# Kernel optimization log

Hardware: AMD Instinct MI355X
Metric: run time of the kernel (lower is better)

The kernel has to match this reference:

```python
import jax, jax.numpy as jnp
import numpy as np

B, L, D, H, HS, V, NL = 8, 513, 512, 8, 64, 513, 6  # head_size = D // H
EPS = 1e-5


def setup_inputs() -> dict:
    key = jax.random.key(0)
    ks = jax.random.split(key, 8)
    s = 0.02
    return {
        "x": jax.random.randint(ks[0], (B, L), 0, V),
        "embed": jax.random.normal(ks[1], (V, D), jnp.float32) * s,
        "pos_embed": jax.random.normal(ks[2], (L, D), jnp.float32) * s,
        "Wq": jax.random.normal(ks[3], (NL, H, D, HS), jnp.float32) * s,
        "Wk": jax.random.normal(ks[4], (NL, H, D, HS), jnp.float32) * s,
        "Wv": jax.random.normal(ks[5], (NL, H, D, HS), jnp.float32) * s,
        "ln1_g": jnp.ones((NL, D), jnp.float32),
        "ln1_b": jnp.zeros((NL, D), jnp.float32),
        "ln2_g": jnp.ones((NL, D), jnp.float32),
        "ln2_b": jnp.zeros((NL, D), jnp.float32),
        "mlp_W": jax.random.normal(ks[6], (NL, D, D), jnp.float32) * s,
        "mlp_b": jnp.zeros((NL, D), jnp.float32),
        "fc_W": jax.random.normal(ks[7], (D, V), jnp.float32) * s,
        "fc_b": jnp.zeros((V,), jnp.float32),
    }


def _layernorm(x, g, b):
    mu = jnp.mean(x, axis=-1, keepdims=True)
    var = jnp.mean(jnp.square(x - mu), axis=-1, keepdims=True)
    return (x - mu) * jax.lax.rsqrt(var + EPS) * g + b


def reference(x, embed, pos_embed, Wq, Wk, Wv, ln1_g, ln1_b, ln2_g, ln2_b,
              mlp_W, mlp_b, fc_W, fc_b):
    h = embed[x] + pos_embed[None]                       # (B, L, D)
    mask = jnp.tril(jnp.ones((L, L), bool))              # causal tril buffer
    scale = HS ** -0.5
    for i in range(NL):
        xn = _layernorm(h, ln1_g[i], ln1_b[i])
        # all heads batched (original loops per head; same math)
        q = jnp.einsum('bld,hde->bhle', xn, Wq[i])
        k = jnp.einsum('bld,hde->bhle', xn, Wk[i])
        v = jnp.einsum('bld,hde->bhle', xn, Wv[i])
        w = jnp.einsum('bhle,bhme->bhlm', q, k) * scale
        w = jnp.where(mask, w, -jnp.inf)
        w = jax.nn.softmax(w, axis=-1)
        y = jnp.einsum('bhlm,bhme->bhle', w, v)
        y = y.transpose(0, 2, 1, 3).reshape(B, L, D)     # concat heads
        h = y + h
        xn2 = _layernorm(h, ln2_g[i], ln2_b[i])
        h = jax.nn.gelu(xn2 @ mlp_W[i] + mlp_b[i], approximate=False) + h
    return h @ fc_W + fc_b                               # (B, L, V) logits
```

## Files before the change

### kernel.cpp

```cpp
#include <hip/hip_runtime.h>
#include <hip/hip_bf16.h>
#include <math.h>

#define B 8
#define L 513
#define D 512
#define H 8
#define HS 64
#define V 513
#define NL 6
#define BL (B * L)
#define LP 576
#define EPS 1e-5f

typedef __attribute__((ext_vector_type(8))) short bf16x8;
typedef __attribute__((ext_vector_type(4))) float f32x4;

__device__ inline ushort f2b(float f) {
    __hip_bfloat16 h = __float2bfloat16(f);
    return *reinterpret_cast<ushort*>(&h);
}

__global__ __launch_bounds__(256) void embed_k(const int* __restrict__ x,
                                               const float* __restrict__ emb,
                                               const float* __restrict__ pos,
                                               float* __restrict__ hbuf)
{
    int row = blockIdx.x;
    int l   = row % L;
    int tok = x[row];
    const float* er = emb + (size_t)tok * D;
    const float* pr = pos + (size_t)l * D;
    float* hr = hbuf + (size_t)row * D;
    for (int d = threadIdx.x; d < D; d += 256)
        hr[d] = er[d] + pr[d];
}

__global__ __launch_bounds__(256) void ln_k(const float* __restrict__ x,
                                            const float* __restrict__ g,
                                            const float* __restrict__ b,
                                            ushort* __restrict__ o)
{
    const int row = blockIdx.x, tid = threadIdx.x;
    const float* xr = x + (size_t)row * D;
    float v0 = xr[tid], v1 = xr[tid + 256];
    __shared__ float red[256];
    red[tid] = v0 + v1;
    __syncthreads();
    for (int off = 128; off > 0; off >>= 1) {
        if (tid < off) red[tid] += red[tid + off];
        __syncthreads();
    }
    float mu = red[0] * (1.f / D);
    __syncthreads();
    float d0 = v0 - mu, d1 = v1 - mu;
    red[tid] = d0 * d0 + d1 * d1;
    __syncthreads();
    for (int off = 128; off > 0; off >>= 1) {
        if (tid < off) red[tid] += red[tid + off];
        __syncthreads();
    }
    float rs = rsqrtf(red[0] * (1.f / D) + EPS);
    ushort* orow = o + (size_t)row * D;
    orow[tid]       = f2b(d0 * rs * g[tid]       + b[tid]);
    orow[tid + 256] = f2b(d1 * rs * g[tid + 256] + b[tid + 256]);
}

__global__ __launch_bounds__(256) void h2bf_k(const float* __restrict__ h,
                                              ushort* __restrict__ o)
{
    int idx = blockIdx.x * 256 + threadIdx.x;
    float4 f = *(const float4*)(h + (size_t)idx * 4);
    ushort4 u;
    u.x = f2b(f.x); u.y = f2b(f.y); u.z = f2b(f.z); u.w = f2b(f.w);
    *(ushort4*)(o + (size_t)idx * 4) = u;
}

__global__ __launch_bounds__(256) void cvt_qkv_k(const float* __restrict__ Wq,
                                                 const float* __restrict__ Wk,
                                                 const float* __restrict__ Wv,
                                                 ushort* __restrict__ Wp)
{
    const int dc = blockIdx.x;
    const int i  = blockIdx.y / H, h = blockIdx.y % H;
    const int sel = blockIdx.z;
    const float* W = (sel == 0) ? Wq : (sel == 1) ? Wk : Wv;
    const float* src = W + ((size_t)i * H + h) * D * HS + (size_t)dc * 64 * HS;
    __shared__ float T[64][65];
    const int tid = threadIdx.x;
#pragma unroll
    for (int it = 0; it < 4; ++it) {
        int idx = tid + it * 256;
        int r = idx >> 4, e4 = (idx & 15) * 4;
        float4 f = *(const float4*)(src + (size_t)r * HS + e4);
        T[r][e4] = f.x; T[r][e4 + 1] = f.y; T[r][e4 + 2] = f.z; T[r][e4 + 3] = f.w;
    }
    __syncthreads();
    ushort* dst = Wp + (size_t)i * 1536 * 512 + (size_t)(sel * 512 + h * 64) * 512 + dc * 64;
#pragma unroll
    for (int it = 0; it < 4; ++it) {
        int idx = tid + it * 256;
        int e = idx >> 4, d4 = (idx & 15) * 4;
        ushort4 u;
        u.x = f2b(T[d4][e]); u.y = f2b(T[d4 + 1][e]);
        u.z = f2b(T[d4 + 2][e]); u.w = f2b(T[d4 + 3][e]);
        *(ushort4*)(dst + (size_t)e * 512 + d4) = u;
    }
}

__global__ __launch_bounds__(256) void cvt_mlp_k(const float* __restrict__ Wm,
                                                 ushort* __restrict__ Wt)
{
    const int nt = blockIdx.x, kt = blockIdx.y, i = blockIdx.z;
    const float* src = Wm + (size_t)i * D * D;
    __shared__ float T[64][65];
    const int tid = threadIdx.x;
#pragma unroll
    for (int it = 0; it < 4; ++it) {
        int idx = tid + it * 256;
        int r = idx >> 4, e4 = (idx & 15) * 4;
        float4 f = *(const float4*)(src + (size_t)(kt * 64 + r) * D + nt * 64 + e4);
        T[r][e4] = f.x; T[r][e4 + 1] = f.y; T[r][e4 + 2] = f.z; T[r][e4 + 3] = f.w;
    }
    __syncthreads();
    ushort* dst = Wt + (size_t)i * D * D + (size_t)(nt * 64) * D + kt * 64;
#pragma unroll
    for (int it = 0; it < 4; ++it) {
        int idx = tid + it * 256;
        int e = idx >> 4, k4 = (idx & 15) * 4;
        ushort4 u;
        u.x = f2b(T[k4][e]); u.y = f2b(T[k4 + 1][e]);
        u.z = f2b(T[k4 + 2][e]); u.w = f2b(T[k4 + 3][e]);
        *(ushort4*)(dst + (size_t)e * D + k4) = u;
    }
}

__global__ __launch_bounds__(256) void cvt_fc_k(const float* __restrict__ Wf,
                                                ushort* __restrict__ Wt)
{
    const int nt = blockIdx.x, kt = blockIdx.y;
    __shared__ float T[64][65];
    const int tid = threadIdx.x;
#pragma unroll
    for (int it = 0; it < 4; ++it) {
        int idx = tid + it * 256;
        int r = idx >> 4, e4 = (idx & 15) * 4;
#pragma unroll
        for (int j = 0; j < 4; ++j) {
            int n = nt * 64 + e4 + j;
            T[r][e4 + j] = (n < V) ? Wf[(size_t)(kt * 64 + r) * V + n] : 0.f;
        }
    }
    __syncthreads();
    ushort* dst = Wt + (size_t)(nt * 64) * 512 + kt * 64;
#pragma unroll
    for (int it = 0; it < 4; ++it) {
        int idx = tid + it * 256;
        int e = idx >> 4, k4 = (idx & 15) * 4;
        ushort4 u;
        u.x = f2b(T[k4][e]); u.y = f2b(T[k4 + 1][e]);
        u.z = f2b(T[k4 + 2][e]); u.w = f2b(T[k4 + 3][e]);
        *(ushort4*)(dst + (size_t)e * 512 + k4) = u;
    }
}

template <int MODE>
__global__ __launch_bounds__(256) void mgemm_k(const ushort* __restrict__ A,
                                               const ushort* __restrict__ Bt,
                                               const float* __restrict__ bias,
                                               void* __restrict__ o0,
                                               void* __restrict__ o1,
                                               void* __restrict__ o2)
{
    __shared__ ushort As[64][72];
    __shared__ ushort Bs[64][72];
    const int tid  = threadIdx.x;
    const int wave = tid >> 6, lane = tid & 63;
    const int row0 = blockIdx.y * 64;
    const int col0 = blockIdx.x * 64;
    const int wr = (wave >> 1) * 32, wc = (wave & 1) * 32;
    const int frow = lane & 15;
    const int kb   = lane >> 4;

    f32x4 acc[2][2] = {};

    for (int k0 = 0; k0 < 512; k0 += 64) {
#pragma unroll
        for (int it = 0; it < 2; ++it) {
            int idx = tid + it * 256;
            int r = idx >> 3, kc = idx & 7;
            uint4 av = make_uint4(0u, 0u, 0u, 0u);
            if (row0 + r < BL)
                av = *(const uint4*)(A + (size_t)(row0 + r) * 512 + k0 + kc * 8);
            *(uint4*)&As[r][kc * 8] = av;
            uint4 bv = *(const uint4*)(Bt + (size_t)(col0 + r) * 512 + k0 + kc * 8);
            *(uint4*)&Bs[r][kc * 8] = bv;
        }
        __syncthreads();
#pragma unroll
        for (int ks = 0; ks < 2; ++ks) {
            bf16x8 a[2], b[2];
#pragma unroll
            for (int f = 0; f < 2; ++f) {
                a[f] = *(const bf16x8*)&As[wr + f * 16 + frow][ks * 32 + kb * 8];
                b[f] = *(const bf16x8*)&Bs[wc + f * 16 + frow][ks * 32 + kb * 8];
            }
#pragma unroll
            for (int fi = 0; fi < 2; ++fi)
#pragma unroll
                for (int fj = 0; fj < 2; ++fj)
                    acc[fi][fj] = __builtin_amdgcn_mfma_f32_16x16x32_bf16(
                        a[fi], b[fj], acc[fi][fj], 0, 0, 0);
        }
        __syncthreads();
    }

    const int rbase = row0 + wr + (lane >> 4) * 4;
    const int cbase = col0 + wc + (lane & 15);
#pragma unroll
    for (int fi = 0; fi < 2; ++fi) {
#pragma unroll
        for (int fj = 0; fj < 2; ++fj) {
            const int c = cbase + fj * 16;
#pragma unroll
            for (int rg = 0; rg < 4; ++rg) {
                const int r = rbase + fi * 16 + rg;
                if (r >= BL) continue;
                float val = acc[fi][fj][rg];
                if (MODE == 0) {
                    int buf = c >> 9, cc = c & 511;
                    int b_ = r / L, l = r % L;
                    int head = cc >> 6, e = cc & 63;
                    int bh = b_ * H + head;
                    if (buf == 0)
                        ((ushort*)o0)[((size_t)bh * L + l) * HS + e] = f2b(val);
                    else if (buf == 1)
                        ((ushort*)o1)[((size_t)bh * L + l) * HS + e] = f2b(val);
                    else
                        ((ushort*)o2)[((size_t)bh * HS + e) * LP + l] = f2b(val);
                } else if (MODE == 1) {
                    float xv = val + bias[c];
                    float gl = 0.5f * xv * (1.f + erff(xv * 0.70710678118654752f));
                    ((float*)o0)[(size_t)r * D + c] = gl + ((float*)o0)[(size_t)r * D + c];
                } else {
                    if (c < V) ((float*)o0)[(size_t)r * V + c] = val + bias[c];
                }
            }
        }
    }
}

__global__ __launch_bounds__(256) void fattn_k(const ushort* __restrict__ qb,
                                               const ushort* __restrict__ kb,
                                               const ushort* __restrict__ vT,
                                               float* __restrict__ hbuf)
{
    __shared__ ushort Qs[64][72];
    __shared__ ushort Ks[64][72];
    __shared__ ushort Vs[64][72];
    __shared__ ushort Ps[64][72];

    const int bx  = blockIdx.x;
    const int bh  = bx / 9;
    const int qt  = 8 - (bx % 9);
    const int q0  = qt * 64;
    const int tid = threadIdx.x;
    const int wave = tid >> 6, lane = tid & 63;
    const int lg = lane >> 4, li = lane & 15;
    const int wq = wave * 16;

#pragma unroll
    for (int it = 0; it < 2; ++it) {
        int idx = tid + it * 256;
        int r = idx >> 3, c8 = (idx & 7) * 8;
        int qr = q0 + r;
        uint4 val = make_uint4(0u, 0u, 0u, 0u);
        if (qr < L) val = *(const uint4*)(qb + ((size_t)bh * L + qr) * HS + c8);
        *(uint4*)&Qs[r][c8] = val;
    }

    float m_run[4], l_run[4];
    f32x4 accO[4] = {};
#pragma unroll
    for (int rg = 0; rg < 4; ++rg) { m_run[rg] = -INFINITY; l_run[rg] = 0.f; }

    const int n_mt = qt + 1;

    for (int t = 0; t < n_mt; ++t) {
        const int m0 = t * 64;
#pragma unroll
        for (int it = 0; it < 2; ++it) {
            int idx = tid + it * 256;
            int r = idx >> 3, c8 = (idx & 7) * 8;
            int mr = m0 + r;
            uint4 kv = make_uint4(0u, 0u, 0u, 0u);
            if (mr < L) kv = *(const uint4*)(kb + ((size_t)bh * L + mr) * HS + c8);
            *(uint4*)&Ks[r][c8] = kv;
            int mc = m0 + c8;
            uint4 vv = make_uint4(0u, 0u, 0u, 0u);
            if (mc + 7 < L) {
                vv = *(const uint4*)(vT + ((size_t)bh * HS + r) * LP + mc);
            } else {
                ushort tmp[8] = {0, 0, 0, 0, 0, 0, 0, 0};
#pragma unroll
                for (int j2 = 0; j2 < 8; ++j2)
                    if (mc + j2 < L) tmp[j2] = vT[((size_t)bh * HS + r) * LP + mc + j2];
                vv = *(uint4*)tmp;
            }
            *(uint4*)&Vs[r][c8] = vv;
        }
        __syncthreads();

        f32x4 accS[4] = {};
#pragma unroll
        for (int ks = 0; ks < 2; ++ks) {
            bf16x8 a = *(const bf16x8*)&Qs[wq + li][ks * 32 + lg * 8];
#pragma unroll
            for (int j = 0; j < 4; ++j) {
                bf16x8 b = *(const bf16x8*)&Ks[j * 16 + li][ks * 32 + lg * 8];
                accS[j] = __builtin_amdgcn_mfma_f32_16x16x32_bf16(a, b, accS[j], 0, 0, 0);
            }
        }

#pragma unroll
        for (int rg = 0; rg < 4; ++rg) {
            const int qrow = q0 + wq + lg * 4 + rg;
            float sv[4];
            float rmax = -INFINITY;
#pragma unroll
            for (int j = 0; j < 4; ++j) {
                int mcol = m0 + j * 16 + li;
                float s = accS[j][rg] * 0.125f;
                if (mcol > qrow || mcol >= L) s = -INFINITY;
                sv[j] = s;
                rmax = fmaxf(rmax, s);
            }
            rmax = fmaxf(rmax, __shfl_xor(rmax, 1));
            rmax = fmaxf(rmax, __shfl_xor(rmax, 2));
            rmax = fmaxf(rmax, __shfl_xor(rmax, 4));
            rmax = fmaxf(rmax, __shfl_xor(rmax, 8));
            const float mnew = fmaxf(m_run[rg], rmax);
            const float fs = __expf(m_run[rg] - mnew);
            float psum = 0.f;
#pragma unroll
            for (int j = 0; j < 4; ++j) {
                float p = __expf(sv[j] - mnew);
                psum += p;
                Ps[wq + lg * 4 + rg][j * 16 + li] = f2b(p);
            }
            psum += __shfl_xor(psum, 1);
            psum += __shfl_xor(psum, 2);
            psum += __shfl_xor(psum, 4);
            psum += __shfl_xor(psum, 8);
            l_run[rg] = l_run[rg] * fs + psum;
            m_run[rg] = mnew;
#pragma unroll
            for (int j = 0; j < 4; ++j) accO[j][rg] *= fs;
        }

#pragma unroll
        for (int ks = 0; ks < 2; ++ks) {
            bf16x8 a = *(const bf16x8*)&Ps[wq + li][ks * 32 + lg * 8];
#pragma unroll
            for (int j = 0; j < 4; ++j) {
                bf16x8 b = *(const bf16x8*)&Vs[j * 16 + li][ks * 32 + lg * 8];
                accO[j] = __builtin_amdgcn_mfma_f32_16x16x32_bf16(a, b, accO[j], 0, 0, 0);
            }
        }
        __syncthreads();
    }

    const int b_ = bh / H, hh = bh % H;
#pragma unroll
    for (int rg = 0; rg < 4; ++rg) {
        const int qrow = q0 + wq + lg * 4 + rg;
        if (qrow >= L) continue;
        const float inv = 1.f / l_run[rg];
        float* dst = hbuf + ((size_t)b_ * L + qrow) * D + hh * HS;
#pragma unroll
        for (int j = 0; j < 4; ++j)
            dst[j * 16 + li] += accO[j][rg] * inv;
    }
}

extern "C" void kernel_launch(void* const* d_in, const int* in_sizes, int n_in,
                              void* d_out, int out_size, void* d_ws, size_t ws_size,
                              hipStream_t stream)
{
    const int*   x    = (const int*)d_in[0];
    const float* emb  = (const float*)d_in[1];
    const float* pos  = (const float*)d_in[2];
    const float* Wq   = (const float*)d_in[3];
    const float* Wk   = (const float*)d_in[4];
    const float* Wv   = (const float*)d_in[5];
    const float* ln1g = (const float*)d_in[6];
    const float* ln1b = (const float*)d_in[7];
    const float* ln2g = (const float*)d_in[8];
    const float* ln2b = (const float*)d_in[9];
    const float* mlpW = (const float*)d_in[10];
    const float* mlpb = (const float*)d_in[11];
    const float* fcW  = (const float*)d_in[12];
    const float* fcb  = (const float*)d_in[13];
    float* out = (float*)d_out;

    char* ws = (char*)d_ws;
    float*  h   = (float*)ws;    ws += (size_t)BL * D * 4;
    ushort* qb  = (ushort*)ws;   ws += (size_t)BL * D * 2;
    ushort* kb  = (ushort*)ws;   ws += (size_t)BL * D * 2;
    ushort* vT  = (ushort*)ws;   ws += (size_t)B * H * HS * LP * 2;
    ushort* xnb = (ushort*)ws;   ws += (size_t)BL * D * 2;
    ushort* hb  = (ushort*)ws;   ws += (size_t)BL * D * 2;
    ushort* Wp  = (ushort*)ws;   ws += (size_t)NL * 1536 * 512 * 2;
    ushort* Wtm = (ushort*)ws;   ws += (size_t)NL * D * D * 2;
    ushort* Wtf = (ushort*)ws;   ws += (size_t)576 * 512 * 2;

    cvt_qkv_k<<<dim3(8, NL * H, 3), 256, 0, stream>>>(Wq, Wk, Wv, Wp);
    cvt_mlp_k<<<dim3(8, 8, NL), 256, 0, stream>>>(mlpW, Wtm);
    cvt_fc_k<<<dim3(9, 8), 256, 0, stream>>>(fcW, Wtf);

    embed_k<<<BL, 256, 0, stream>>>(x, emb, pos, h);

    for (int i = 0; i < NL; ++i) {
        ln_k<<<BL, 256, 0, stream>>>(h, ln1g + i * D, ln1b + i * D, xnb);
        mgemm_k<0><<<dim3(24, 65), 256, 0, stream>>>(
            xnb, Wp + (size_t)i * 1536 * 512, nullptr, qb, kb, vT);
        fattn_k<<<B * H * 9, 256, 0, stream>>>(qb, kb, vT, h);
        ln_k<<<BL, 256, 0, stream>>>(h, ln2g + i * D, ln2b + i * D, xnb);
        mgemm_k<1><<<dim3(8, 65), 256, 0, stream>>>(
            xnb, Wtm + (size_t)i * D * D, mlpb + i * D, h, nullptr, nullptr);
    }
    h2bf_k<<<BL * D / 1024, 256, 0, stream>>>(h, hb);
    mgemm_k<2><<<dim3(9, 65), 256, 0, stream>>>(hb, Wtf, fcb, out, nullptr, nullptr);
}
```

Baseline: 646.0 us.

## Enlarge GEMM tiles to 128x128 with direct-to-LDS loads and swizzle, warp-level layernorm

Measured after the change: 727.2 us. +12.6%, slower.

```diff
diff --git a/kernel.cpp b/kernel.cpp
--- a/kernel.cpp
+++ b/kernel.cpp
@@ -21,6 +21,12 @@
     return *reinterpret_cast<ushort*>(&h);
 }
 
+__device__ inline void gload16(const void* g, void* l) {
+    __builtin_amdgcn_global_load_lds(
+        (const __attribute__((address_space(1))) void*)g,
+        (__attribute__((address_space(3))) void*)l, 16, 0, 0);
+}
+
 __global__ __launch_bounds__(256) void embed_k(const int* __restrict__ x,
                                                const float* __restrict__ emb,
                                                const float* __restrict__ pos,
@@ -36,44 +42,37 @@
         hr[d] = er[d] + pr[d];
 }
 
-__global__ __launch_bounds__(256) void ln_k(const float* __restrict__ x,
-                                            const float* __restrict__ g,
-                                            const float* __restrict__ b,
-                                            ushort* __restrict__ o)
-{
-    const int row = blockIdx.x, tid = threadIdx.x;
-    const float* xr = x + (size_t)row * D;
-    float v0 = xr[tid], v1 = xr[tid + 256];
-    __shared__ float red[256];
-    red[tid] = v0 + v1;
-    __syncthreads();
-    for (int off = 128; off > 0; off >>= 1) {
-        if (tid < off) red[tid] += red[tid + off];
-        __syncthreads();
-    }
-    float mu = red[0] * (1.f / D);
-    __syncthreads();
-    float d0 = v0 - mu, d1 = v1 - mu;
-    red[tid] = d0 * d0 + d1 * d1;
-    __syncthreads();
-    for (int off = 128; off > 0; off >>= 1) {
-        if (tid < off) red[tid] += red[tid + off];
-        __syncthreads();
-    }
-    float rs = rsqrtf(red[0] * (1.f / D) + EPS);
-    ushort* orow = o + (size_t)row * D;
-    orow[tid]       = f2b(d0 * rs * g[tid]       + b[tid]);
-    orow[tid + 256] = f2b(d1 * rs * g[tid + 256] + b[tid + 256]);
-}
-
-__global__ __launch_bounds__(256) void h2bf_k(const float* __restrict__ h,
-                                              ushort* __restrict__ o)
-{
-    int idx = blockIdx.x * 256 + threadIdx.x;
-    float4 f = *(const float4*)(h + (size_t)idx * 4);
-    ushort4 u;
-    u.x = f2b(f.x); u.y = f2b(f.y); u.z = f2b(f.z); u.w = f2b(f.w);
-    *(ushort4*)(o + (size_t)idx * 4) = u;
+__global__ __launch_bounds__(64) void ln_k(const float* __restrict__ x,
+                                           const float* __restrict__ g,
+                                           const float* __restrict__ b,
+                                           ushort* __restrict__ o)
+{
+    const int row = blockIdx.x, lane = threadIdx.x;
+    const float* xr = x + (size_t)row * D + lane * 8;
+    float4 v0 = *(const float4*)xr;
+    float4 v1 = *(const float4*)(xr + 4);
+    float s = v0.x + v0.y + v0.z + v0.w + v1.x + v1.y + v1.z + v1.w;
+#pragma unroll
+    for (int off = 1; off < 64; off <<= 1) s += __shfl_xor(s, off);
+    const float mu = s * (1.f / D);
+    float d0 = v0.x - mu, d1 = v0.y - mu, d2 = v0.z - mu, d3 = v0.w - mu;
+    float d4 = v1.x - mu, d5 = v1.y - mu, d6 = v1.z - mu, d7 = v1.w - mu;
+    float ss = d0*d0 + d1*d1 + d2*d2 + d3*d3 + d4*d4 + d5*d5 + d6*d6 + d7*d7;
+#pragma unroll
+    for (int off = 1; off < 64; off <<= 1) ss += __shfl_xor(ss, off);
+    const float rs = rsqrtf(ss * (1.f / D) + EPS);
+    const float* gp = g + lane * 8;
+    const float* bp = b + lane * 8;
+    float4 g0 = *(const float4*)gp, g1 = *(const float4*)(gp + 4);
+    float4 b0 = *(const float4*)bp, b1 = *(const float4*)(bp + 4);
+    ushort4 u0, u1;
+    u0.x = f2b(d0 * rs * g0.x + b0.x); u0.y = f2b(d1 * rs * g0.y + b0.y);
+    u0.z = f2b(d2 * rs * g0.z + b0.z); u0.w = f2b(d3 * rs * g0.w + b0.w);
+    u1.x = f2b(d4 * rs * g1.x + b1.x); u1.y = f2b(d5 * rs * g1.y + b1.y);
+    u1.z = f2b(d6 * rs * g1.z + b1.z); u1.w = f2b(d7 * rs * g1.w + b1.w);
+    ushort* orow = o + (size_t)row * D + lane * 8;
+    *(ushort4*)orow       = u0;
+    *(ushort4*)(orow + 4) = u1;
 }
 
 __global__ __launch_bounds__(256) void cvt_qkv_k(const float* __restrict__ Wq,
@@ -172,43 +171,45 @@
                                                void* __restrict__ o1,
                                                void* __restrict__ o2)
 {
-    __shared__ ushort As[64][72];
-    __shared__ ushort Bs[64][72];
+    __shared__ ushort As[128 * 64] __attribute__((aligned(16)));
+    __shared__ ushort Bs[128 * 64] __attribute__((aligned(16)));
     const int tid  = threadIdx.x;
     const int wave = tid >> 6, lane = tid & 63;
-    const int row0 = blockIdx.y * 64;
-    const int col0 = blockIdx.x * 64;
-    const int wr = (wave >> 1) * 32, wc = (wave & 1) * 32;
+    const int row0 = blockIdx.y * 128;
+    const int col0 = blockIdx.x * 128;
+    const int wr = (wave >> 1) * 64, wc = (wave & 1) * 64;
     const int frow = lane & 15;
     const int kb   = lane >> 4;
 
-    f32x4 acc[2][2] = {};
+    const int ci0 = wave * 4 * 64 + lane;
+
+    f32x4 acc[4][4] = {};
 
     for (int k0 = 0; k0 < 512; k0 += 64) {
 #pragma unroll
-        for (int it = 0; it < 2; ++it) {
-            int idx = tid + it * 256;
-            int r = idx >> 3, kc = idx & 7;
-            uint4 av = make_uint4(0u, 0u, 0u, 0u);
-            if (row0 + r < BL)
-                av = *(const uint4*)(A + (size_t)(row0 + r) * 512 + k0 + kc * 8);
-            *(uint4*)&As[r][kc * 8] = av;
-            uint4 bv = *(const uint4*)(Bt + (size_t)(col0 + r) * 512 + k0 + kc * 8);
-            *(uint4*)&Bs[r][kc * 8] = bv;
+        for (int i = 0; i < 4; ++i) {
+            int ci = ci0 + i * 64;
+            int r = ci >> 3, kc = ci & 7;
+            int sc = (kc ^ (r & 7)) * 8;
+            gload16(A  + (size_t)(row0 + r) * 512 + k0 + sc, &As[(wave * 4 + i) * 512]);
+            gload16(Bt + (size_t)(col0 + r) * 512 + k0 + sc, &Bs[(wave * 4 + i) * 512]);
         }
         __syncthreads();
 #pragma unroll
         for (int ks = 0; ks < 2; ++ks) {
-            bf16x8 a[2], b[2];
-#pragma unroll
-            for (int f = 0; f < 2; ++f) {
-                a[f] = *(const bf16x8*)&As[wr + f * 16 + frow][ks * 32 + kb * 8];
-                b[f] = *(const bf16x8*)&Bs[wc + f * 16 + frow][ks * 32 + kb * 8];
-            }
-#pragma unroll
-            for (int fi = 0; fi < 2; ++fi)
-#pragma unroll
-                for (int fj = 0; fj < 2; ++fj)
+            bf16x8 a[4], b[4];
+            const int g = ks * 4 + kb;
+#pragma unroll
+            for (int f = 0; f < 4; ++f) {
+                const int ra = wr + f * 16 + frow;
+                a[f] = *(const bf16x8*)&As[ra * 64 + ((g ^ (ra & 7)) * 8)];
+                const int rb = wc + f * 16 + frow;
+                b[f] = *(const bf16x8*)&Bs[rb * 64 + ((g ^ (rb & 7)) * 8)];
+            }
+#pragma unroll
+            for (int fi = 0; fi < 4; ++fi)
+#pragma unroll
+                for (int fj = 0; fj < 4; ++fj)
                     acc[fi][fj] = __builtin_amdgcn_mfma_f32_16x16x32_bf16(
                         a[fi], b[fj], acc[fi][fj], 0, 0, 0);
         }
@@ -218,9 +219,9 @@
     const int rbase = row0 + wr + (lane >> 4) * 4;
     const int cbase = col0 + wc + (lane & 15);
 #pragma unroll
-    for (int fi = 0; fi < 2; ++fi) {
-#pragma unroll
-        for (int fj = 0; fj < 2; ++fj) {
+    for (int fi = 0; fi < 4; ++fi) {
+#pragma unroll
+        for (int fj = 0; fj < 4; ++fj) {
             const int c = cbase + fj * 16;
 #pragma unroll
             for (int rg = 0; rg < 4; ++rg) {
@@ -242,6 +243,11 @@
                     float xv = val + bias[c];
                     float gl = 0.5f * xv * (1.f + erff(xv * 0.70710678118654752f));
                     ((float*)o0)[(size_t)r * D + c] = gl + ((float*)o0)[(size_t)r * D + c];
+                } else if (MODE == 3) {
+                    float xv = val + bias[c];
+                    float gl = 0.5f * xv * (1.f + erff(xv * 0.70710678118654752f));
+                    float res = ((const float*)o1)[(size_t)r * D + c];
+                    ((ushort*)o0)[(size_t)r * D + c] = f2b(gl + res);
                 } else {
                     if (c < V) ((float*)o0)[(size_t)r * V + c] = val + bias[c];
                 }
@@ -406,29 +412,32 @@
     char* ws = (char*)d_ws;
     float*  h   = (float*)ws;    ws += (size_t)BL * D * 4;
     ushort* qb  = (ushort*)ws;   ws += (size_t)BL * D * 2;
-    ushort* kb  = (ushort*)ws;   ws += (size_t)BL * D * 2;
+    ushort* kbuf= (ushort*)ws;   ws += (size_t)BL * D * 2;
     ushort* vT  = (ushort*)ws;   ws += (size_t)B * H * HS * LP * 2;
     ushort* xnb = (ushort*)ws;   ws += (size_t)BL * D * 2;
     ushort* hb  = (ushort*)ws;   ws += (size_t)BL * D * 2;
     ushort* Wp  = (ushort*)ws;   ws += (size_t)NL * 1536 * 512 * 2;
     ushort* Wtm = (ushort*)ws;   ws += (size_t)NL * D * D * 2;
-    ushort* Wtf = (ushort*)ws;   ws += (size_t)576 * 512 * 2;
+    ushort* Wtf = (ushort*)ws;   ws += (size_t)640 * 512 * 2;
 
     cvt_qkv_k<<<dim3(8, NL * H, 3), 256, 0, stream>>>(Wq, Wk, Wv, Wp);
     cvt_mlp_k<<<dim3(8, 8, NL), 256, 0, stream>>>(mlpW, Wtm);
-    cvt_fc_k<<<dim3(9, 8), 256, 0, stream>>>(fcW, Wtf);
+    cvt_fc_k<<<dim3(10, 8), 256, 0, stream>>>(fcW, Wtf);
 
     embed_k<<<BL, 256, 0, stream>>>(x, emb, pos, h);
 
     for (int i = 0; i < NL; ++i) {
-        ln_k<<<BL, 256, 0, stream>>>(h, ln1g + i * D, ln1b + i * D, xnb);
-        mgemm_k<0><<<dim3(24, 65), 256, 0, stream>>>(
-            xnb, Wp + (size_t)i * 1536 * 512, nullptr, qb, kb, vT);
-        fattn_k<<<B * H * 9, 256, 0, stream>>>(qb, kb, vT, h);
-        ln_k<<<BL, 256, 0, stream>>>(h, ln2g + i * D, ln2b + i * D, xnb);
-        mgemm_k<1><<<dim3(8, 65), 256, 0, stream>>>(
-            xnb, Wtm + (size_t)i * D * D, mlpb + i * D, h, nullptr, nullptr);
-    }
-    h2bf_k<<<BL * D / 1024, 256, 0, stream>>>(h, hb);
-    mgemm_k<2><<<dim3(9, 65), 256, 0, stream>>>(hb, Wtf, fcb, out, nullptr, nullptr);
-}
+        ln_k<<<BL, 64, 0, stream>>>(h, ln1g + i * D, ln1b + i * D, xnb);
+        mgemm_k<0><<<dim3(12, 33), 256, 0, stream>>>(
+            xnb, Wp + (size_t)i * 1536 * 512, nullptr, qb, kbuf, vT);
+        fattn_k<<<B * H * 9, 256, 0, stream>>>(qb, kbuf, vT, h);
+        ln_k<<<BL, 64, 0, stream>>>(h, ln2g + i * D, ln2b + i * D, xnb);
+        if (i < NL - 1)
+            mgemm_k<1><<<dim3(4, 33), 256, 0, stream>>>(
+                xnb, Wtm + (size_t)i * D * D, mlpb + i * D, h, nullptr, nullptr);
+        else
+            mgemm_k<3><<<dim3(4, 33), 256, 0, stream>>>(
+                xnb, Wtm + (size_t)i * D * D, mlpb + i * D, hb, h, nullptr);
+    }
+    mgemm_k<2><<<dim3(5, 33), 256, 0, stream>>>(hb, Wtf, fcb, out, nullptr, nullptr);
+}
```
